# Optimization experiments

Hardware: AMD Instinct MI355X
Metric: run time of the kernel (lower is better)

## Reference

```python
import jax, jax.numpy as jnp
import numpy as np

NUM_HEADS = 16
ROPE_BASE = 10000.0
MAX_POS = 4096


def _rope_tables(head_dim):
    inv_freq = 1.0 / (ROPE_BASE ** (np.arange(0, head_dim, 2, dtype=np.float32) / head_dim))
    freqs = np.arange(MAX_POS, dtype=np.float32)[:, None] * inv_freq[None, :]
    emb = np.concatenate([freqs, freqs], axis=-1)  # [MAX_POS, head_dim]
    return jnp.asarray(np.cos(emb)), jnp.asarray(np.sin(emb))


def _rotate_half(x):
    d = x.shape[-1] // 2
    return jnp.concatenate([-x[..., d:], x[..., :d]], axis=-1)


def _apply_rope(x, pos, cos_t, sin_t):
    # x: [B,H,S,D], pos: [B,S]
    cos = cos_t[pos][:, None]  # [B,1,S,D]
    sin = sin_t[pos][:, None]
    return x * cos + _rotate_half(x) * sin


def setup_inputs() -> dict:
    key = jax.random.key(0)
    ks = jax.random.split(key, 8)
    B, N, M, C = 2, 2048, 2048, 1024
    s = 1.0 / np.sqrt(C)
    return {
        "query": jax.random.normal(ks[0], (B, N, C), jnp.float32),
        "key": jax.random.normal(ks[1], (B, M, C), jnp.float32),
        "query_pos": jnp.broadcast_to(jnp.arange(N, dtype=jnp.int32), (B, N)),
        "key_pos": jnp.broadcast_to(jnp.arange(M, dtype=jnp.int32), (B, M)),
        "Wq": jax.random.normal(ks[2], (C, C), jnp.float32) * s,
        "bq": jnp.zeros((C,), jnp.float32),
        "Wk": jax.random.normal(ks[3], (C, C), jnp.float32) * s,
        "Wv": jax.random.normal(ks[4], (C, C), jnp.float32) * s,
        "bv": jnp.zeros((C,), jnp.float32),
        "Wo": jax.random.normal(ks[5], (C, C), jnp.float32) * s,
        "bo": jnp.zeros((C,), jnp.float32),
    }


def reference(query, key, query_pos, key_pos, Wq, bq, Wk, Wv, bv, Wo, bo):
    B, N, C = query.shape
    M = key.shape[1]
    H = NUM_HEADS
    D = C // H
    scale = D ** -0.5
    cos_t, sin_t = _rope_tables(D)

    value = key  # value defaults to key
    identity = query

    q = (query @ Wq.T + bq).reshape(B, N, H, D).transpose(0, 2, 1, 3)
    k = (key @ Wk.T).reshape(B, M, H, D).transpose(0, 2, 1, 3)
    v = (value @ Wv.T + bv).reshape(B, M, H, D).transpose(0, 2, 1, 3)

    q = _apply_rope(q, query_pos, cos_t, sin_t)
    k = _apply_rope(k, key_pos, cos_t, sin_t)

    attn = jnp.einsum('bhnd,bhmd->bhnm', q, k) * scale
    attn = jax.nn.softmax(attn, axis=-1)
    x = jnp.einsum('bhnm,bhmd->bhnd', attn, v)  # [B,H,N,D]
    x = x.transpose(0, 2, 1, 3).reshape(B, N, C)
    x = x @ Wo.T + bo
    return x + identity
```

## Files before the change

### kernel.cpp

```cpp
#include <hip/hip_runtime.h>
#include <hip/hip_bf16.h>
#include <stdint.h>

#define B_ 2
#define N_ 2048
#define M_ 2048
#define C_ 1024
#define H_ 16
#define D_ 64

typedef __attribute__((ext_vector_type(8))) short s16x8;
typedef __attribute__((ext_vector_type(4))) short s16x4;
typedef __attribute__((ext_vector_type(4))) float f32x4;
typedef __attribute__((ext_vector_type(16))) float f32x16;

__device__ __attribute__((always_inline)) inline short f2b(float f){
    __hip_bfloat16 h = __float2bfloat16(f); short s; __builtin_memcpy(&s, &h, 2); return s;
}
__device__ __attribute__((always_inline)) inline float b2f(short s){
    __hip_bfloat16 h; __builtin_memcpy(&h, &s, 2); return __bfloat162float(h);
}

#define MFMA16(a,b,c) __builtin_amdgcn_mfma_f32_16x16x32_bf16(a,b,c,0,0,0)
#define MFMA32(a,b,c) __builtin_amdgcn_mfma_f32_32x32x16_bf16(a,b,c,0,0,0)

__device__ __attribute__((always_inline)) inline void gl_lds16(const void* g, void* l){
    __builtin_amdgcn_global_load_lds((__attribute__((address_space(1))) void*)g,
                                     (__attribute__((address_space(3))) void*)l, 16, 0, 0);
}
__device__ __attribute__((always_inline)) inline unsigned fbits(float f){
    unsigned u; __builtin_memcpy(&u, &f, 4); return u;
}

__global__ void cvt_all(const float* __restrict__ q, const float* __restrict__ k,
                        const float* __restrict__ wq, const float* __restrict__ wk,
                        const float* __restrict__ wv, const float* __restrict__ wo,
                        short* __restrict__ dst){
    long i = ((long)blockIdx.x * 256 + threadIdx.x) * 8;
    const float* src; long off;
    if      (i <  4194304L){ src = q;  off = i; }
    else if (i <  8388608L){ src = k;  off = i - 4194304L; }
    else if (i <  9437184L){ src = wq; off = i - 8388608L; }
    else if (i < 10485760L){ src = wk; off = i - 9437184L; }
    else if (i < 11534336L){ src = wv; off = i - 10485760L; }
    else                   { src = wo; off = i - 11534336L; }
    float4 a = *(const float4*)(src + off);
    float4 b = *(const float4*)(src + off + 4);
    s16x8 o;
    o[0]=f2b(a.x); o[1]=f2b(a.y); o[2]=f2b(a.z); o[3]=f2b(a.w);
    o[4]=f2b(b.x); o[5]=f2b(b.y); o[6]=f2b(b.z); o[7]=f2b(b.w);
    *(s16x8*)(dst + i) = o;
}

__global__ __launch_bounds__(256, 3) void gemm_qkv(
    const short* __restrict__ qbf, const short* __restrict__ kbf,
    const short* __restrict__ W,
    const float* __restrict__ bq, const float* __restrict__ bv,
    short* __restrict__ qproj, short* __restrict__ kproj, short* __restrict__ vT)
{
    __shared__ short As[128 * 32];
    __shared__ short Bs[128 * 32];
    const int n0 = blockIdx.x * 128, m0 = blockIdx.y * 128;
    const int sel = n0 >> 10;
    const short* A = (sel == 0) ? qbf : kbf;
    const int tid = threadIdx.x, lane = tid & 63, wave = tid >> 6;
    const int quad = lane >> 4, l16 = lane & 15;
    const int wr = (wave >> 1) * 64, wc = (wave & 1) * 64;
    const int srow = lane >> 2, scol = (lane & 3) * 8;

    f32x4 acc[4][4] = {};

    const short* Ag = A + (size_t)(m0 + wave * 32 + srow) * C_ + scol;
    const short* Bg = W + (size_t)(n0 + wave * 32 + srow) * C_ + scol;
    short* lA0 = As + (wave * 32) * 32;
    short* lA1 = As + (wave * 32 + 16) * 32;
    short* lB0 = Bs + (wave * 32) * 32;
    short* lB1 = Bs + (wave * 32 + 16) * 32;

    for (int k0 = 0; k0 < C_; k0 += 32){
        __syncthreads();
        gl_lds16(Ag + k0, lA0);
        gl_lds16(Ag + k0 + 16 * (size_t)C_, lA1);
        gl_lds16(Bg + k0, lB0);
        gl_lds16(Bg + k0 + 16 * (size_t)C_, lB1);
        __syncthreads();
        s16x8 af[4], bfr[4];
        #pragma unroll
        for (int t = 0; t < 4; t++) af[t]  = *(const s16x8*)&As[(wr + t*16 + l16) * 32 + quad * 8];
        #pragma unroll
        for (int t = 0; t < 4; t++) bfr[t] = *(const s16x8*)&Bs[(wc + t*16 + l16) * 32 + quad * 8];
        #pragma unroll
        for (int i = 0; i < 4; i++)
            #pragma unroll
            for (int j = 0; j < 4; j++)
                acc[i][j] = MFMA16(af[i], bfr[j], acc[i][j]);
    }

    if (sel <= 1){
        short* dst = sel ? kproj : qproj;
        const float* bp = sel ? nullptr : bq;
        const int coff = sel << 10;
        #pragma unroll
        for (int j = 0; j < 4; j++){
            int c = n0 + wc + j * 16 + l16 - coff;
            float bb = bp ? bp[c] : 0.0f;
            #pragma unroll
            for (int i = 0; i < 4; i++){
                int row = m0 + wr + i * 16 + quad * 4;
                #pragma unroll
                for (int r = 0; r < 4; r++)
                    dst[(size_t)(row + r) * C_ + c] = f2b(acc[i][j][r] + bb);
            }
        }
    } else {
        #pragma unroll
        for (int j = 0; j < 4; j++){
            int col = n0 - 2048 + wc + j * 16 + l16;
            int h = col >> 6, d = col & 63;
            float bb = bv[col];
            #pragma unroll
            for (int i = 0; i < 4; i++){
                int row = m0 + wr + i * 16 + quad * 4;
                int b = row >> 11, m = row & 2047;
                unsigned u0 = (unsigned)(unsigned short)f2b(acc[i][j][0] + bb) |
                              ((unsigned)(unsigned short)f2b(acc[i][j][1] + bb) << 16);
                unsigned u1 = (unsigned)(unsigned short)f2b(acc[i][j][2] + bb) |
                              ((unsigned)(unsigned short)f2b(acc[i][j][3] + bb) << 16);
                uint2 u; u.x = u0; u.y = u1;
                *(uint2*)&vT[(((size_t)(b * H_ + h)) * D_ + d) * M_ + m] = u;
            }
        }
    }
}

__global__ __launch_bounds__(256, 4) void gemm_out(
    const short* __restrict__ A, const short* __restrict__ W,
    const float* __restrict__ bias, const float* __restrict__ resid,
    float* __restrict__ outf)
{
    __shared__ short As[128 * 32];
    __shared__ short Bs[64 * 32];
    const int n0 = blockIdx.x * 64, m0 = blockIdx.y * 128;
    const int tid = threadIdx.x, lane = tid & 63, wave = tid >> 6;
    const int quad = lane >> 4, l16 = lane & 15;
    const int srow = lane >> 2, scol = (lane & 3) * 8;

    f32x4 acc[2][4] = {};
    const short* Ag = A + (size_t)(m0 + wave * 32 + srow) * C_ + scol;
    const short* Bg = W + (size_t)(n0 + wave * 16 + srow) * C_ + scol;
    short* lA0 = As + (wave * 32) * 32;
    short* lA1 = As + (wave * 32 + 16) * 32;
    short* lB  = Bs + (wave * 16) * 32;

    for (int k0 = 0; k0 < C_; k0 += 32){
        __syncthreads();
        gl_lds16(Ag + k0, lA0);
        gl_lds16(Ag + k0 + 16 * (size_t)C_, lA1);
        gl_lds16(Bg + k0, lB);
        __syncthreads();
        s16x8 af[2], bfr[4];
        #pragma unroll
        for (int t = 0; t < 2; t++) af[t]  = *(const s16x8*)&As[(wave*32 + t*16 + l16) * 32 + quad * 8];
        #pragma unroll
        for (int t = 0; t < 4; t++) bfr[t] = *(const s16x8*)&Bs[(t*16 + l16) * 32 + quad * 8];
        #pragma unroll
        for (int i = 0; i < 2; i++)
            #pragma unroll
            for (int j = 0; j < 4; j++)
                acc[i][j] = MFMA16(af[i], bfr[j], acc[i][j]);
    }

    #pragma unroll
    for (int j = 0; j < 4; j++){
        int c = n0 + j * 16 + l16;
        float bb = bias[c];
        #pragma unroll
        for (int i = 0; i < 2; i++){
            int row = m0 + wave * 32 + i * 16 + quad * 4;
            #pragma unroll
            for (int r = 0; r < 4; r++){
                size_t idx = (size_t)(row + r) * C_ + c;
                outf[idx] = acc[i][j][r] + bb + resid[idx];
            }
        }
    }
}

__global__ void rope_k(short* __restrict__ k, const int* __restrict__ kpos){
    int t = blockIdx.x * blockDim.x + threadIdx.x;
    int i = t & 31;
    int h = (t >> 5) & (H_ - 1);
    int row = t >> 9;
    int pos = kpos[row];
    short* base = k + (size_t)row * C_ + h * D_;
    float x1 = b2f(base[i]), x2 = b2f(base[i + 32]);
    float invf = exp2f((float)i * (-13.287712379549449f / 32.0f));
    float f = (float)pos * invf;
    float c = __cosf(f), s = __sinf(f);
    base[i]      = f2b(x1 * c - x2 * s);
    base[i + 32] = f2b(x2 * c + x1 * s);
}

__global__ __launch_bounds__(256, 3) void flash_attn(
    const short* __restrict__ q, const short* __restrict__ k,
    const short* __restrict__ vt, short* __restrict__ o,
    const int* __restrict__ qpos)
{
    __shared__ short smem[17152];
    const int b = blockIdx.y >> 4, h = blockIdx.y & 15;
    const int n0 = blockIdx.x * 128;
    const int tid = threadIdx.x, lane = tid & 63, wave = tid >> 6;
    const int hi = lane >> 5, l32 = lane & 31;
    const int wq = wave & 1, kq = wave >> 1;

    s16x8 qf[2][4];
    const float fac = 0.18033688011112042f;
    #pragma unroll
    for (int qt = 0; qt < 2; qt++){
        int qrow = n0 + wq * 64 + qt * 32 + l32;
        const short* qg = &q[((size_t)(b * N_ + qrow)) * C_ + h * D_];
        float pos = (float)qpos[b * N_ + qrow];
        s16x8 raw[4];
        #pragma unroll
        for (int c = 0; c < 4; c++) raw[c] = *(const s16x8*)&qg[c * 16 + hi * 8];
        #pragma unroll
        for (int c = 0; c < 2; c++){
            s16x8 olo, ohi8;
            #pragma unroll
            for (int j = 0; j < 8; j++){
                int irot = c * 16 + hi * 8 + j;
                float invf = exp2f((float)irot * (-13.287712379549449f / 32.0f));
                float ang = pos * invf;
                float cs = __cosf(ang), sn = __sinf(ang);
                float x1 = b2f(raw[c][j]), x2 = b2f(raw[c + 2][j]);
                olo[j]  = f2b((x1 * cs - x2 * sn) * fac);
                ohi8[j] = f2b((x2 * cs + x1 * sn) * fac);
            }
            qf[qt][c] = olo; qf[qt][c + 2] = ohi8;
        }
    }

    const short* kg = k  + (size_t)(b * M_) * C_ + h * D_;
    const short* vg = vt + ((size_t)(b * H_ + h)) * D_ * M_;
    const int sr8 = lane >> 3;
    const int g8  = (lane & 7) ^ sr8;

    f32x16 zero16 = {};
    f32x16 oacc[2][2] = {zero16, zero16, zero16, zero16};
    float lacc[2] = {0.f, 0.f};

    #pragma unroll
    for (int i = 0; i < 2; i++){
        int base = wave * 16 + i * 8;
        gl_lds16(kg + (size_t)(base + sr8) * C_ + g8 * 8, &smem[base * 64]);
        gl_lds16(vg + (size_t)(base + sr8) * M_ + g8 * 8, &smem[8192 + base * 64]);
    }

    for (int st = 0; st < 32; st++){
        const int p = st & 1, pn = p ^ 1;
        __syncthreads();
        if (st < 31){
            #pragma unroll
            for (int i = 0; i < 2; i++){
                int base = wave * 16 + i * 8;
                gl_lds16(kg + (size_t)((st + 1) * 64 + base + sr8) * C_ + g8 * 8,
                         &smem[pn * 4096 + base * 64]);
                gl_lds16(vg + (size_t)(base + sr8) * M_ + (st + 1) * 64 + g8 * 8,
                         &smem[8192 + pn * 4096 + base * 64]);
            }
        }
        const short* Kp = &smem[p * 4096];
        const short* Vp = &smem[8192 + p * 4096];

        const int r7 = l32 & 7;
        const int kbase = (kq * 32 + l32) * 64;
        s16x8 kf[4];
        #pragma unroll
        for (int c = 0; c < 4; c++)
            kf[c] = *(const s16x8*)&Kp[kbase + ((2 * c + hi) ^ r7) * 8];

        s16x8 pf[2][2];
        #pragma unroll
        for (int qt = 0; qt < 2; qt++){
            f32x16 sv = {};
            #pragma unroll
            for (int c = 0; c < 4; c++)
                sv = MFMA32(kf[c], qf[qt][c], sv);
            float ls = 0.f;
            unsigned pb[8];
            #pragma unroll
            for (int g = 0; g < 4; g++){
                float p0 = __builtin_amdgcn_exp2f(sv[4*g+0]);
                float p1 = __builtin_amdgcn_exp2f(sv[4*g+1]);
                float p2 = __builtin_amdgcn_exp2f(sv[4*g+2]);
                float p3 = __builtin_amdgcn_exp2f(sv[4*g+3]);
                ls += (p0 + p1) + (p2 + p3);
                pb[2*g]   = __builtin_amdgcn_perm(fbits(p1), fbits(p0), 0x07060302);
                pb[2*g+1] = __builtin_amdgcn_perm(fbits(p3), fbits(p2), 0x07060302);
            }
            lacc[qt] += ls;
            unsigned s0 = hi ? pb[0] : pb[2];
            unsigned s1 = hi ? pb[1] : pb[3];
            unsigned s2 = hi ? pb[4] : pb[6];
            unsigned s3 = hi ? pb[5] : pb[7];
            unsigned r0 = (unsigned)__shfl_xor((int)s0, 32);
            unsigned r1 = (unsigned)__shfl_xor((int)s1, 32);
            unsigned r2 = (unsigned)__shfl_xor((int)s2, 32);
            unsigned r3 = (unsigned)__shfl_xor((int)s3, 32);
            union { unsigned u[4]; s16x8 v; } f0, f1;
            f0.u[0] = hi ? r0 : pb[0];
            f0.u[1] = hi ? r1 : pb[1];
            f0.u[2] = hi ? pb[2] : r0;
            f0.u[3] = hi ? pb[3] : r1;
            f1.u[0] = hi ? r2 : pb[4];
            f1.u[1] = hi ? r3 : pb[5];
            f1.u[2] = hi ? pb[6] : r2;
            f1.u[3] = hi ? pb[7] : r3;
            pf[qt][0] = f0.v; pf[qt][1] = f1.v;
        }

        s16x8 vf[2][2];
        #pragma unroll
        for (int dt = 0; dt < 2; dt++){
            const int vbase = (dt * 32 + l32) * 64;
            #pragma unroll
            for (int c = 0; c < 2; c++)
                vf[dt][c] = *(const s16x8*)&Vp[vbase + ((4 * kq + 2 * c + hi) ^ r7) * 8];
        }
        #pragma unroll
        for (int qt = 0; qt < 2; qt++)
            #pragma unroll
            for (int dt = 0; dt < 2; dt++)
                #pragma unroll
                for (int c = 0; c < 2; c++)
                    oacc[qt][dt] = MFMA32(pf[qt][c], vf[dt][c], oacc[qt][dt]);
    }

    __syncthreads();

    float* LO   = (float*)smem;
    float* Lsum = (float*)&smem[16640];
    float* Linv = (float*)&smem[16896];

    float l0[2];
    #pragma unroll
    for (int qt = 0; qt < 2; qt++)
        l0[qt] = lacc[qt] + __shfl_xor(lacc[qt], 32);

    if (kq == 1){
        #pragma unroll
        for (int qt = 0; qt < 2; qt++)
            Lsum[wq * 64 + qt * 32 + l32] = l0[qt];
        #pragma unroll
        for (int qt = 0; qt < 2; qt++)
            #pragma unroll
            for (int dt = 0; dt < 2; dt++)
                #pragma unroll
                for (int e = 0; e < 16; e++){
                    int qrow = wq * 64 + qt * 32 + (e & 3) + 8 * (e >> 2) + 4 * hi;
                    LO[qrow * 65 + dt * 32 + l32] = oacc[qt][dt][e];
                }
    }
    __syncthreads();
    if (kq == 0){
        #pragma unroll
        for (int qt = 0; qt < 2; qt++){
            float lt = l0[qt] + Lsum[wq * 64 + qt * 32 + l32];
            Linv[wq * 64 + qt * 32 + l32] = 1.0f / lt;
        }
        asm volatile("s_waitcnt lgkmcnt(0)" ::: "memory");
        #pragma unroll
        for (int qt = 0; qt < 2; qt++)
            #pragma unroll
            for (int dt = 0; dt < 2; dt++)
                #pragma unroll
                for (int e = 0; e < 16; e++){
                    int qrow = wq * 64 + qt * 32 + (e & 3) + 8 * (e >> 2) + 4 * hi;
                    float val = (oacc[qt][dt][e] + LO[qrow * 65 + dt * 32 + l32]) * Linv[qrow];
                    o[((size_t)(b * N_ + n0 + qrow)) * C_ + h * D_ + dt * 32 + l32] = f2b(val);
                }
    }
}

extern "C" void kernel_launch(void* const* d_in, const int* in_sizes, int n_in,
                              void* d_out, int out_size, void* d_ws, size_t ws_size,
                              hipStream_t stream) {
    const float* query = (const float*)d_in[0];
    const float* key   = (const float*)d_in[1];
    const int*   qpos  = (const int*)d_in[2];
    const int*   kpos  = (const int*)d_in[3];
    const float* Wq    = (const float*)d_in[4];
    const float* bq    = (const float*)d_in[5];
    const float* Wk    = (const float*)d_in[6];
    const float* Wv    = (const float*)d_in[7];
    const float* bv    = (const float*)d_in[8];
    const float* Wo    = (const float*)d_in[9];
    const float* bo    = (const float*)d_in[10];
    float* out = (float*)d_out;

    const size_t E4M = (size_t)4 * 1024 * 1024;
    const size_t E1M = (size_t)1024 * 1024;
    short* ws    = (short*)d_ws;
    short* qbf   = ws;
    short* kbf   = qbf   + E4M;
    short* wqkvb = kbf   + E4M;
    short* wob   = wqkvb + 3 * E1M;
    short* qproj = wob   + E1M;
    short* kproj = qproj + E4M;
    short* vT    = kproj + E4M;
    short* attn  = qbf;

    cvt_all<<<6144, 256, 0, stream>>>(query, key, Wq, Wk, Wv, Wo, ws);

    gemm_qkv<<<dim3(24, 32), 256, 0, stream>>>(qbf, kbf, wqkvb, bq, bv,
                                               qproj, kproj, vT);

    rope_k<<<(B_ * M_ * H_ * 32) / 256, 256, 0, stream>>>(kproj, kpos);

    flash_attn<<<dim3(16, 32), 256, 0, stream>>>(qproj, kproj, vT, attn, qpos);

    gemm_out<<<dim3(16, 32), 256, 0, stream>>>(attn, wob, bo, query, out);
}
```

Baseline: 220.6 us.

## Use 8 waves per attention block and register-staged padded LDS loads

The flash attention kernel now runs 512 threads with 8 waves, each owning 32 query rows instead of 64. This halves per-wave accumulator state and raises wave-level parallelism. K/V tile staging also changes: the direct global-to-LDS swizzled copies are replaced by register-prefetched global loads written into padded rows (stride 68). The padding avoids bank conflicts but costs more LDS, split 8-byte LDS accesses, and an extra register stage.

```diff
diff --git a/kernel.cpp b/kernel.cpp
--- a/kernel.cpp
+++ b/kernel.cpp
@@ -201,23 +201,22 @@
     base[i + 32] = f2b(x2 * c + x1 * s);
 }
 
-__global__ __launch_bounds__(256, 3) void flash_attn(
+__global__ __launch_bounds__(512, 2) void flash_attn(
     const short* __restrict__ q, const short* __restrict__ k,
     const short* __restrict__ vt, short* __restrict__ o,
     const int* __restrict__ qpos)
 {
-    __shared__ short smem[17152];
+    __shared__ short smem[17920];
     const int b = blockIdx.y >> 4, h = blockIdx.y & 15;
     const int n0 = blockIdx.x * 128;
     const int tid = threadIdx.x, lane = tid & 63, wave = tid >> 6;
     const int hi = lane >> 5, l32 = lane & 31;
-    const int wq = wave & 1, kq = wave >> 1;
-
-    s16x8 qf[2][4];
+    const int wq = wave & 3, kq = wave >> 2;
+
+    s16x8 qf[4];
     const float fac = 0.18033688011112042f;
-    #pragma unroll
-    for (int qt = 0; qt < 2; qt++){
-        int qrow = n0 + wq * 64 + qt * 32 + l32;
+    {
+        int qrow = n0 + wq * 32 + l32;
         const short* qg = &q[((size_t)(b * N_ + qrow)) * C_ + h * D_];
         float pos = (float)qpos[b * N_ + qrow];
         s16x8 raw[4];
@@ -236,69 +235,77 @@
                 olo[j]  = f2b((x1 * cs - x2 * sn) * fac);
                 ohi8[j] = f2b((x2 * cs + x1 * sn) * fac);
             }
-            qf[qt][c] = olo; qf[qt][c + 2] = ohi8;
+            qf[c] = olo; qf[c + 2] = ohi8;
         }
     }
 
     const short* kg = k  + (size_t)(b * M_) * C_ + h * D_;
     const short* vg = vt + ((size_t)(b * H_ + h)) * D_ * M_;
-    const int sr8 = lane >> 3;
-    const int g8  = (lane & 7) ^ sr8;
+    const int srow0 = tid >> 3, sseg = (tid & 7) * 8;
+
+    union V8 { s16x8 v; uint2 u[2]; };
+    V8 kreg, vreg;
+
+    kreg.v = *(const s16x8*)&kg[(size_t)srow0 * C_ + sseg];
+    vreg.v = *(const s16x8*)&vg[(size_t)srow0 * M_ + sseg];
+    {
+        short* kd = &smem[srow0 * 68 + sseg];
+        *(uint2*)kd = kreg.u[0]; *(uint2*)(kd + 4) = kreg.u[1];
+        short* vd = &smem[8704 + srow0 * 68 + sseg];
+        *(uint2*)vd = vreg.u[0]; *(uint2*)(vd + 4) = vreg.u[1];
+    }
+    kreg.v = *(const s16x8*)&kg[(size_t)(64 + srow0) * C_ + sseg];
+    vreg.v = *(const s16x8*)&vg[(size_t)srow0 * M_ + 64 + sseg];
 
     f32x16 zero16 = {};
-    f32x16 oacc[2][2] = {zero16, zero16, zero16, zero16};
-    float lacc[2] = {0.f, 0.f};
-
-    #pragma unroll
-    for (int i = 0; i < 2; i++){
-        int base = wave * 16 + i * 8;
-        gl_lds16(kg + (size_t)(base + sr8) * C_ + g8 * 8, &smem[base * 64]);
-        gl_lds16(vg + (size_t)(base + sr8) * M_ + g8 * 8, &smem[8192 + base * 64]);
-    }
+    f32x16 oacc[2] = {zero16, zero16};
+    float lacc = 0.f;
 
     for (int st = 0; st < 32; st++){
         const int p = st & 1, pn = p ^ 1;
         __syncthreads();
         if (st < 31){
-            #pragma unroll
-            for (int i = 0; i < 2; i++){
-                int base = wave * 16 + i * 8;
-                gl_lds16(kg + (size_t)((st + 1) * 64 + base + sr8) * C_ + g8 * 8,
-                         &smem[pn * 4096 + base * 64]);
-                gl_lds16(vg + (size_t)(base + sr8) * M_ + (st + 1) * 64 + g8 * 8,
-                         &smem[8192 + pn * 4096 + base * 64]);
-            }
-        }
-        const short* Kp = &smem[p * 4096];
-        const short* Vp = &smem[8192 + p * 4096];
-
-        const int r7 = l32 & 7;
-        const int kbase = (kq * 32 + l32) * 64;
+            short* kd = &smem[pn * 4352 + srow0 * 68 + sseg];
+            *(uint2*)kd = kreg.u[0]; *(uint2*)(kd + 4) = kreg.u[1];
+            short* vd = &smem[8704 + pn * 4352 + srow0 * 68 + sseg];
+            *(uint2*)vd = vreg.u[0]; *(uint2*)(vd + 4) = vreg.u[1];
+        }
+        if (st < 30){
+            kreg.v = *(const s16x8*)&kg[((size_t)((st + 2) * 64 + srow0)) * C_ + sseg];
+            vreg.v = *(const s16x8*)&vg[(size_t)srow0 * M_ + (st + 2) * 64 + sseg];
+        }
+        const short* Kp = &smem[p * 4352];
+        const short* Vp = &smem[8704 + p * 4352];
+
         s16x8 kf[4];
         #pragma unroll
+        for (int c = 0; c < 4; c++){
+            const short* a = &Kp[(kq * 32 + l32) * 68 + c * 16 + hi * 8];
+            kf[c] = __builtin_shufflevector(*(const s16x4*)a, *(const s16x4*)(a + 4),
+                                            0,1,2,3,4,5,6,7);
+        }
+
+        f32x16 sv = {};
+        #pragma unroll
         for (int c = 0; c < 4; c++)
-            kf[c] = *(const s16x8*)&Kp[kbase + ((2 * c + hi) ^ r7) * 8];
-
-        s16x8 pf[2][2];
-        #pragma unroll
-        for (int qt = 0; qt < 2; qt++){
-            f32x16 sv = {};
-            #pragma unroll
-            for (int c = 0; c < 4; c++)
-                sv = MFMA32(kf[c], qf[qt][c], sv);
-            float ls = 0.f;
-            unsigned pb[8];
-            #pragma unroll
-            for (int g = 0; g < 4; g++){
-                float p0 = __builtin_amdgcn_exp2f(sv[4*g+0]);
-                float p1 = __builtin_amdgcn_exp2f(sv[4*g+1]);
-                float p2 = __builtin_amdgcn_exp2f(sv[4*g+2]);
-                float p3 = __builtin_amdgcn_exp2f(sv[4*g+3]);
-                ls += (p0 + p1) + (p2 + p3);
-                pb[2*g]   = __builtin_amdgcn_perm(fbits(p1), fbits(p0), 0x07060302);
-                pb[2*g+1] = __builtin_amdgcn_perm(fbits(p3), fbits(p2), 0x07060302);
-            }
-            lacc[qt] += ls;
+            sv = MFMA32(kf[c], qf[c], sv);
+
+        float ls = 0.f;
+        unsigned pb[8];
+        #pragma unroll
+        for (int g = 0; g < 4; g++){
+            float p0 = __builtin_amdgcn_exp2f(sv[4*g+0]);
+            float p1 = __builtin_amdgcn_exp2f(sv[4*g+1]);
+            float p2 = __builtin_amdgcn_exp2f(sv[4*g+2]);
+            float p3 = __builtin_amdgcn_exp2f(sv[4*g+3]);
+            ls += (p0 + p1) + (p2 + p3);
+            pb[2*g]   = __builtin_amdgcn_perm(fbits(p1), fbits(p0), 0x07060302);
+            pb[2*g+1] = __builtin_amdgcn_perm(fbits(p3), fbits(p2), 0x07060302);
+        }
+        lacc += ls;
+
+        s16x8 pf[2];
+        {
             unsigned s0 = hi ? pb[0] : pb[2];
             unsigned s1 = hi ? pb[1] : pb[3];
             unsigned s2 = hi ? pb[4] : pb[6];
@@ -316,69 +323,57 @@
             f1.u[1] = hi ? r3 : pb[5];
             f1.u[2] = hi ? pb[6] : r2;
             f1.u[3] = hi ? pb[7] : r3;
-            pf[qt][0] = f0.v; pf[qt][1] = f1.v;
+            pf[0] = f0.v; pf[1] = f1.v;
         }
 
         s16x8 vf[2][2];
         #pragma unroll
-        for (int dt = 0; dt < 2; dt++){
-            const int vbase = (dt * 32 + l32) * 64;
+        for (int dt = 0; dt < 2; dt++)
+            #pragma unroll
+            for (int c = 0; c < 2; c++){
+                const short* a = &Vp[(dt * 32 + l32) * 68 + kq * 32 + c * 16 + hi * 8];
+                vf[dt][c] = __builtin_shufflevector(*(const s16x4*)a, *(const s16x4*)(a + 4),
+                                                    0,1,2,3,4,5,6,7);
+            }
+        #pragma unroll
+        for (int dt = 0; dt < 2; dt++)
             #pragma unroll
             for (int c = 0; c < 2; c++)
-                vf[dt][c] = *(const s16x8*)&Vp[vbase + ((4 * kq + 2 * c + hi) ^ r7) * 8];
-        }
-        #pragma unroll
-        for (int qt = 0; qt < 2; qt++)
-            #pragma unroll
-            for (int dt = 0; dt < 2; dt++)
-                #pragma unroll
-                for (int c = 0; c < 2; c++)
-                    oacc[qt][dt] = MFMA32(pf[qt][c], vf[dt][c], oacc[qt][dt]);
+                oacc[dt] = MFMA32(pf[c], vf[dt][c], oacc[dt]);
     }
 
     __syncthreads();
 
     float* LO   = (float*)smem;
-    float* Lsum = (float*)&smem[16640];
-    float* Linv = (float*)&smem[16896];
-
-    float l0[2];
-    #pragma unroll
-    for (int qt = 0; qt < 2; qt++)
-        l0[qt] = lacc[qt] + __shfl_xor(lacc[qt], 32);
+    float* Lsum = (float*)&smem[17408];
+    float* Linv = (float*)&smem[17664];
+
+    float l0 = lacc + __shfl_xor(lacc, 32);
+    const int qbase = wq * 32;
 
     if (kq == 1){
-        #pragma unroll
-        for (int qt = 0; qt < 2; qt++)
-            Lsum[wq * 64 + qt * 32 + l32] = l0[qt];
-        #pragma unroll
-        for (int qt = 0; qt < 2; qt++)
-            #pragma unroll
-            for (int dt = 0; dt < 2; dt++)
-                #pragma unroll
-                for (int e = 0; e < 16; e++){
-                    int qrow = wq * 64 + qt * 32 + (e & 3) + 8 * (e >> 2) + 4 * hi;
-                    LO[qrow * 65 + dt * 32 + l32] = oacc[qt][dt][e];
-                }
+        Lsum[qbase + l32] = l0;
+        #pragma unroll
+        for (int dt = 0; dt < 2; dt++)
+            #pragma unroll
+            for (int e = 0; e < 16; e++){
+                int qrow = qbase + (e & 3) + 8 * (e >> 2) + 4 * hi;
+                LO[qrow * 65 + dt * 32 + l32] = oacc[dt][e];
+            }
     }
     __syncthreads();
     if (kq == 0){
-        #pragma unroll
-        for (int qt = 0; qt < 2; qt++){
-            float lt = l0[qt] + Lsum[wq * 64 + qt * 32 + l32];
-            Linv[wq * 64 + qt * 32 + l32] = 1.0f / lt;
-        }
+        float lt = l0 + Lsum[qbase + l32];
+        Linv[qbase + l32] = 1.0f / lt;
         asm volatile("s_waitcnt lgkmcnt(0)" ::: "memory");
         #pragma unroll
-        for (int qt = 0; qt < 2; qt++)
-            #pragma unroll
-            for (int dt = 0; dt < 2; dt++)
-                #pragma unroll
-                for (int e = 0; e < 16; e++){
-                    int qrow = wq * 64 + qt * 32 + (e & 3) + 8 * (e >> 2) + 4 * hi;
-                    float val = (oacc[qt][dt][e] + LO[qrow * 65 + dt * 32 + l32]) * Linv[qrow];
-                    o[((size_t)(b * N_ + n0 + qrow)) * C_ + h * D_ + dt * 32 + l32] = f2b(val);
-                }
+        for (int dt = 0; dt < 2; dt++)
+            #pragma unroll
+            for (int e = 0; e < 16; e++){
+                int qrow = qbase + (e & 3) + 8 * (e >> 2) + 4 * hi;
+                float val = (oacc[dt][e] + LO[qrow * 65 + dt * 32 + l32]) * Linv[qrow];
+                o[((size_t)(b * N_ + n0 + qrow)) * C_ + h * D_ + dt * 32 + l32] = f2b(val);
+            }
     }
 }
 
@@ -417,7 +412,7 @@
 
     rope_k<<<(B_ * M_ * H_ * 32) / 256, 256, 0, stream>>>(kproj, kpos);
 
-    flash_attn<<<dim3(16, 32), 256, 0, stream>>>(qproj, kproj, vT, attn, qpos);
+    flash_attn<<<dim3(16, 32), 512, 0, stream>>>(qproj, kproj, vT, attn, qpos);
 
     gemm_out<<<dim3(16, 32), 256, 0, stream>>>(attn, wob, bo, query, out);
 }
```

New measurement: 214.5 us. -2.7%, faster.
